# Kernel tuning notes

Measured on AMD Instinct MI355X. Metric: run time of the kernel, lower is better.

## Reference

```python
import jax, jax.numpy as jnp
import numpy as np

NEG = -1.0e9  # masked_fill value from the original module

def setup_inputs() -> dict:
    key = jax.random.key(0)
    kq, kk, kv, km = jax.random.split(key, 4)
    B, H, S, D = 4, 16, 2048, 64
    Q = jax.random.normal(kq, (B, H, S, D), dtype=jnp.float32)
    K = jax.random.normal(kk, (B, H, S, D), dtype=jnp.float32)
    V = jax.random.normal(kv, (B, H, S, D), dtype=jnp.float32)
    # boolean mask, True = masked out (broadcast over batch and heads)
    mask = jax.random.randint(km, (1, 1, S, S), 0, 2).astype(jnp.bool_)
    return {"Q": Q, "K": K, "V": V, "mask": mask}

def reference(Q, K, V, mask):
    d_k = K.shape[-1]
    scale = 1.0 / jnp.sqrt(jnp.asarray(d_k, dtype=Q.dtype))
    # [B,H,S,S] attention scores
    scores = jnp.einsum("bhqd,bhkd->bhqk", Q, K) * scale
    scores = jnp.where(mask, jnp.asarray(NEG, dtype=scores.dtype), scores)
    weights = jax.nn.softmax(scores, axis=-1)
    # dropout is identity in eval mode (self.training == False)
    return jnp.einsum("bhqk,bhkd->bhqd", weights, V)
```

## Files before the change

kernel.cpp:

```cpp
#include <hip/hip_runtime.h>
#include <stdint.h>

#define SQ 2048
#define DH 64

typedef __attribute__((ext_vector_type(8))) short bf16x8;
typedef __attribute__((ext_vector_type(4))) short bf16x4;
typedef __attribute__((ext_vector_type(4))) float f32x4;

static __device__ __forceinline__ unsigned short f2bf_rne(float x) {
  union { float f; uint32_t u; } v; v.f = x;
  uint32_t u = v.u;
  return (unsigned short)((u + 0x7FFFu + ((u >> 16) & 1u)) >> 16);
}

static __device__ __forceinline__ uint32_t pack_hi(float a, float b) {
  uint32_t au = __float_as_uint(a), bu = __float_as_uint(b);
#if __has_builtin(__builtin_amdgcn_perm)
  return __builtin_amdgcn_perm(bu, au, 0x07060302u);
#else
  return (bu & 0xFFFF0000u) | (au >> 16);
#endif
}

static __device__ __forceinline__ uint32_t pack_sel(float a, float b, uint32_t sel) {
#if __has_builtin(__builtin_amdgcn_perm)
  return __builtin_amdgcn_perm(__float_as_uint(b), __float_as_uint(a), sel);
#else
  uint32_t r = 0;
  uint64_t src = ((uint64_t)__float_as_uint(b) << 32) | __float_as_uint(a);
  for (int i = 0; i < 4; ++i) {
    uint32_t sb = (sel >> (8 * i)) & 0xFF;
    uint32_t byte = (sb < 8) ? (uint32_t)((src >> (8 * sb)) & 0xFF) : 0u;
    r |= byte << (8 * i);
  }
  return r;
#endif
}

static __device__ __forceinline__ float fast_exp2(float x) {
#if __has_builtin(__builtin_amdgcn_exp2f)
  return __builtin_amdgcn_exp2f(x);
#else
  return exp2f(x);
#endif
}

#if __has_builtin(__builtin_amdgcn_mfma_f32_16x16x16_bf16)
#define MFMA_PV(a, b, c) __builtin_amdgcn_mfma_f32_16x16x16_bf16((a), (b), (c), 0, 0, 0)
#else
#define MFMA_PV(a, b, c) __builtin_amdgcn_mfma_f32_16x16x16bf16_1k((a), (b), (c), 0, 0, 0)
#endif

__global__ __launch_bounds__(256) void pack_all(const float* __restrict__ K,
                                                const float* __restrict__ V,
                                                const int* __restrict__ mask,
                                                uint4* __restrict__ pk,
                                                uint2* __restrict__ pv,
                                                uint2* __restrict__ pm) {
  const int t = threadIdx.x;
  if (blockIdx.x < 2048) {
    __shared__ uint32_t Vw[64][33];
    const int bt = blockIdx.x;
    {
      const float* src = K + (size_t)bt * 64 * DH;
      uint4* dst = pk + (size_t)bt * 512;
#pragma unroll
      for (int j = 0; j < 2; ++j) {
        int i = t + j * 256;
        int kk = i >> 3, cp = i & 7;
        int c = cp ^ (kk & 7);
        const float4* s4 = (const float4*)(src + (size_t)kk * DH + c * 8);
        float4 a = s4[0], b = s4[1];
        uint4 w;
        w.x = pack_hi(a.x, a.y); w.y = pack_hi(a.z, a.w);
        w.z = pack_hi(b.x, b.y); w.w = pack_hi(b.z, b.w);
        dst[i] = w;
      }
    }
    {
      const float* src = V + (size_t)bt * 64 * DH;
#pragma unroll
      for (int half = 0; half < 2; ++half) {
        int kp = (t >> 4) + half * 16;
        int d4 = (t & 15) * 4;
        float4 a = *(const float4*)(src + (size_t)(2 * kp) * DH + d4);
        float4 b = *(const float4*)(src + (size_t)(2 * kp + 1) * DH + d4);
        Vw[d4 + 0][kp] = pack_hi(a.x, b.x);
        Vw[d4 + 1][kp] = pack_hi(a.y, b.y);
        Vw[d4 + 2][kp] = pack_hi(a.z, b.z);
        Vw[d4 + 3][kp] = pack_hi(a.w, b.w);
      }
      __syncthreads();
      uint2* dst = pv + (size_t)bt * 1024;
#pragma unroll
      for (int j = 0; j < 4; ++j) {
        int o = t + j * 256;
        int d = o >> 4, up = o & 15;
        int u = up ^ (d & 15);
        uint2 w;
        w.x = Vw[d][2 * u]; w.y = Vw[d][2 * u + 1];
        dst[o] = w;
      }
    }
  } else {
    __shared__ uint2 Lm[16][17];
    const int bid = blockIdx.x - 2048;
    const int qb = bid >> 5, gb = bid & 31;
    {
      int qq = t >> 4, gg = t & 15;
      int4 m = *(const int4*)(mask + (size_t)(qb * 16 + qq) * SQ + (gb * 64 + gg * 4));
      uint2 w;
      w.x = (m.x ? 0x00000C0Cu : 0x00000302u) | (m.y ? 0x0C0C0000u : 0x07060000u);
      w.y = (m.z ? 0x00000C0Cu : 0x00000302u) | (m.w ? 0x0C0C0000u : 0x07060000u);
      Lm[gg][qq] = w;
    }
    __syncthreads();
    {
      int gg = t >> 4, qq = t & 15;
      pm[(size_t)(gb * 16 + gg) * 2048 + qb * 16 + qq] = Lm[gg][qq];
    }
  }
}

__global__ void pack_mask_kernel(const int* __restrict__ mask,
                                 unsigned long long* __restrict__ bits) {
  const int lane = threadIdx.x & 63;
  const int gw = (blockIdx.x * blockDim.x + threadIdx.x) >> 6;
  const int nw = (gridDim.x * blockDim.x) >> 6;
  for (int w = gw; w < SQ * SQ / 64; w += nw) {
    int v = mask[(size_t)w * 64 + lane];
    unsigned long long b = __ballot(v != 0);
    if (lane == 0) bits[(size_t)(w & 31) * SQ + (w >> 5)] = b;
  }
}

__global__ __launch_bounds__(256, 2) void attn3(
    const uint4* __restrict__ pk, const uint4* __restrict__ pv,
    const uint2* __restrict__ pm, const float* __restrict__ Qg,
    float* __restrict__ Og) {
  __shared__ __align__(16) uint8_t smem[32768];

  const int id = blockIdx.x;
  const int bh = id & 63;
  const int qblk = id >> 6;
  const int t = threadIdx.x;
  const int wave = t >> 6, lane = t & 63, col = lane & 15, quad = lane >> 4;

  const float* Qb = Qg + (size_t)bh * SQ * DH;
  float* Ob = Og + (size_t)bh * SQ * DH;
  const uint4* pkb = pk + (size_t)bh * 32 * 512;
  const uint4* pvb = pv + (size_t)bh * 32 * 512;
  const int q0 = qblk * 256 + wave * 64;

  const float QSCALE = 0.18033688011112042f;
  bf16x8 qf[4][2];
#pragma unroll
  for (int s = 0; s < 4; ++s) {
    int q = q0 + s * 16 + col;
#pragma unroll
    for (int j = 0; j < 2; ++j) {
      const float4* p = (const float4*)(Qb + (size_t)q * DH + j * 32 + quad * 8);
      float4 a = p[0], b = p[1];
      bf16x8 f;
      f[0] = (short)f2bf_rne(a.x * QSCALE); f[1] = (short)f2bf_rne(a.y * QSCALE);
      f[2] = (short)f2bf_rne(a.z * QSCALE); f[3] = (short)f2bf_rne(a.w * QSCALE);
      f[4] = (short)f2bf_rne(b.x * QSCALE); f[5] = (short)f2bf_rne(b.y * QSCALE);
      f[6] = (short)f2bf_rne(b.z * QSCALE); f[7] = (short)f2bf_rne(b.w * QSCALE);
      qf[s][j] = f;
    }
  }

  const unsigned ka0 = col * 128 + ((quad ^ (col & 7)) * 16);
  const unsigned ka1 = col * 128 + (((4 + quad) ^ (col & 7)) * 16);
  unsigned va[4];
#pragma unroll
  for (int kt = 0; kt < 4; ++kt)
    va[kt] = 16384u + col * 128 + (((kt * 4 + quad) ^ col) * 8);
  const unsigned stK = t * 16;
  const unsigned stV = 16384u + t * 16;
  const char* pmt = (const char*)pm + (size_t)(quad * 2048 + q0 + col) * 8;

  f32x4 acc[4][4];
  f32x4 accl[4];
#pragma unroll
  for (int s = 0; s < 4; ++s) {
#pragma unroll
    for (int dt = 0; dt < 4; ++dt)
#pragma unroll
      for (int r = 0; r < 4; ++r) acc[s][dt][r] = 0.0f;
#pragma unroll
    for (int r = 0; r < 4; ++r) accl[s][r] = 0.0f;
  }
  bf16x4 vones;
  vones[0] = (short)0x3F80; vones[1] = (short)0x3F80;
  vones[2] = (short)0x3F80; vones[3] = (short)0x3F80;
  const f32x4 fz = {0.0f, 0.0f, 0.0f, 0.0f};

  {
    uint4 k0 = pkb[t], k1 = pkb[t + 256];
    uint4 v0 = pvb[t], v1 = pvb[t + 256];
    *(uint4*)(smem + stK) = k0; *(uint4*)(smem + stK + 4096) = k1;
    *(uint4*)(smem + stV) = v0; *(uint4*)(smem + stV + 4096) = v1;
  }
  unsigned buf = 0;

  for (int tile = 0; tile < 32; ++tile) {
    __syncthreads();
    const int tn = (tile < 31) ? tile + 1 : 31;

    const uint4* pkt = pkb + (size_t)tn * 512;
    const uint4* pvt = pvb + (size_t)tn * 512;
    uint4 k0 = pkt[t], k1 = pkt[t + 256];
    uint4 v0 = pvt[t], v1 = pvt[t + 256];

#pragma unroll
    for (int kt = 0; kt < 4; ++kt) {
      const bf16x8 kf0 = *(const bf16x8*)(smem + buf + kt * 2048 + ka0);
      const bf16x8 kf1 = *(const bf16x8*)(smem + buf + kt * 2048 + ka1);
      uint2 mw[4];
#pragma unroll
      for (int s = 0; s < 4; ++s)
        mw[s] = *(const uint2*)(pmt + (size_t)kt * 65536 + s * 128);

      uint32_t pf[4][2];
#pragma unroll
      for (int s = 0; s < 4; ++s) {
        f32x4 st = __builtin_amdgcn_mfma_f32_16x16x32_bf16(kf0, qf[s][0], fz, 0, 0, 0);
        st = __builtin_amdgcn_mfma_f32_16x16x32_bf16(kf1, qf[s][1], st, 0, 0, 0);
        float p0 = fast_exp2(st[0]), p1 = fast_exp2(st[1]);
        float p2 = fast_exp2(st[2]), p3 = fast_exp2(st[3]);
        pf[s][0] = pack_sel(p0, p1, mw[s].x);
        pf[s][1] = pack_sel(p2, p3, mw[s].y);
      }

      union { uint2 u2; bf16x4 v; } vf[4];
#pragma unroll
      for (int dt = 0; dt < 4; ++dt)
        vf[dt].u2 = *(const uint2*)(smem + buf + va[kt] + dt * 2048);
#pragma unroll
      for (int s = 0; s < 4; ++s) {
        union { uint32_t u[2]; bf16x4 v; } pw;
        pw.u[0] = pf[s][0]; pw.u[1] = pf[s][1];
        accl[s] = MFMA_PV(vones, pw.v, accl[s]);
#pragma unroll
        for (int dt = 0; dt < 4; ++dt)
          acc[s][dt] = MFMA_PV(vf[dt].v, pw.v, acc[s][dt]);
      }
    }

    const unsigned ob = buf ^ 8192u;
    *(uint4*)(smem + ob + stK) = k0; *(uint4*)(smem + ob + stK + 4096) = k1;
    *(uint4*)(smem + ob + stV) = v0; *(uint4*)(smem + ob + stV + 4096) = v1;
    buf = ob;
    pmt += 262144;
  }

#pragma unroll
  for (int s = 0; s < 4; ++s) {
    float inv = 1.0f / accl[s][0];
    int q = q0 + s * 16 + col;
    float* orow = Ob + (size_t)q * DH;
#pragma unroll
    for (int dt = 0; dt < 4; ++dt) {
      float4 o;
      o.x = acc[s][dt][0] * inv;
      o.y = acc[s][dt][1] * inv;
      o.z = acc[s][dt][2] * inv;
      o.w = acc[s][dt][3] * inv;
      *(float4*)(orow + dt * 16 + quad * 4) = o;
    }
  }
}

__global__ __launch_bounds__(512, 4) void attn_fb(
    const float* __restrict__ Qg, const float* __restrict__ Kg,
    const float* __restrict__ Vg, const unsigned long long* __restrict__ mbits,
    const int* __restrict__ mraw, float* __restrict__ Og) {
  __shared__ __align__(16) unsigned short Klds[2][64][72];
  __shared__ __align__(16) uint32_t Vtlds[2][64][36];
  const int id = blockIdx.x;
  const int bh = id & 63;
  const int qblk = id >> 6;
  const int t = threadIdx.x;
  const int wave = t >> 6, lane = t & 63, col = lane & 15, quad = lane >> 4;
  const float* Qb = Qg + (size_t)bh * SQ * DH;
  const float* Kb = Kg + (size_t)bh * SQ * DH;
  const float* Vb = Vg + (size_t)bh * SQ * DH;
  float* Ob = Og + (size_t)bh * SQ * DH;
  const int q0 = qblk * 256 + wave * 32;
  const int skk = t >> 3, sd8 = (t & 7) * 8, skp = t >> 4, sd4 = (t & 15) * 4;
  const float QSCALE = 0.18033688011112042f;
  bf16x8 qf[2][2];
#pragma unroll
  for (int s = 0; s < 2; ++s) {
    int q = q0 + s * 16 + col;
#pragma unroll
    for (int j = 0; j < 2; ++j) {
      const float4* p = (const float4*)(Qb + (size_t)q * DH + j * 32 + quad * 8);
      float4 a = p[0], b = p[1];
      bf16x8 f;
      f[0] = (short)f2bf_rne(a.x * QSCALE); f[1] = (short)f2bf_rne(a.y * QSCALE);
      f[2] = (short)f2bf_rne(a.z * QSCALE); f[3] = (short)f2bf_rne(a.w * QSCALE);
      f[4] = (short)f2bf_rne(b.x * QSCALE); f[5] = (short)f2bf_rne(b.y * QSCALE);
      f[6] = (short)f2bf_rne(b.z * QSCALE); f[7] = (short)f2bf_rne(b.w * QSCALE);
      qf[s][j] = f;
    }
  }
  f32x4 acc[2][4]; f32x4 accl[2];
#pragma unroll
  for (int s = 0; s < 2; ++s) {
#pragma unroll
    for (int dt = 0; dt < 4; ++dt)
#pragma unroll
      for (int r = 0; r < 4; ++r) acc[s][dt][r] = 0.0f;
#pragma unroll
    for (int r = 0; r < 4; ++r) accl[s][r] = 0.0f;
  }
  bf16x4 vones;
  vones[0] = (short)0x3F80; vones[1] = (short)0x3F80;
  vones[2] = (short)0x3F80; vones[3] = (short)0x3F80;
  const f32x4 fz = {0.0f, 0.0f, 0.0f, 0.0f};
  auto load_mask = [&](int ti, unsigned long long m[2]) {
    if (mbits) {
#pragma unroll
      for (int s = 0; s < 2; ++s)
        m[s] = mbits[(size_t)ti * SQ + (q0 + s * 16 + col)];
    } else {
#pragma unroll
      for (int s = 0; s < 2; ++s) {
        int q = q0 + s * 16 + col;
        unsigned long long mm = 0;
#pragma unroll
        for (int j = 0; j < 4; ++j) {
          int4 mi = *(const int4*)(mraw + (size_t)q * SQ + ti * 64 + j * 16 + quad * 4);
          unsigned long long nib = (unsigned long long)((mi.x != 0) | ((mi.y != 0) << 1) |
                                                        ((mi.z != 0) << 2) | ((mi.w != 0) << 3));
          mm |= nib << (j * 16 + quad * 4);
        }
        m[s] = mm;
      }
    }
  };
  {
    const float4* kp = (const float4*)(Kb + (size_t)skk * DH + sd8);
    float4 k0 = kp[0], k1 = kp[1];
    const float* va = Vb + (size_t)(skp * 2) * DH + sd4;
    float4 v0 = *(const float4*)va, v1 = *(const float4*)(va + DH);
    uint4 kw;
    kw.x = pack_hi(k0.x, k0.y); kw.y = pack_hi(k0.z, k0.w);
    kw.z = pack_hi(k1.x, k1.y); kw.w = pack_hi(k1.z, k1.w);
    *(uint4*)&Klds[0][skk][sd8] = kw;
    Vtlds[0][sd4 + 0][skp] = pack_hi(v0.x, v1.x);
    Vtlds[0][sd4 + 1][skp] = pack_hi(v0.y, v1.y);
    Vtlds[0][sd4 + 2][skp] = pack_hi(v0.z, v1.z);
    Vtlds[0][sd4 + 3][skp] = pack_hi(v0.w, v1.w);
  }
  unsigned long long mcur[2];
  load_mask(0, mcur);
  for (int tile = 0; tile < 32; ++tile) {
    __syncthreads();
    const int cb = tile & 1, nb = cb ^ 1;
    const int tn = (tile + 1 < 32) ? tile + 1 : tile;
    const int kkn = tn * 64;
    const float4* kp = (const float4*)(Kb + (size_t)(kkn + skk) * DH + sd8);
    float4 k0 = kp[0], k1 = kp[1];
    const float* va = Vb + (size_t)(kkn + skp * 2) * DH + sd4;
    float4 v0 = *(const float4*)va;
    float4 v1 = *(const float4*)(va + DH);
    unsigned long long mnxt[2];
    load_mask(tn, mnxt);
    uint32_t pfw[2][4][2];
#pragma unroll
    for (int kt = 0; kt < 4; ++kt) {
      const bf16x8 kf0 = *(const bf16x8*)&Klds[cb][kt * 16 + col][quad * 8];
      const bf16x8 kf1 = *(const bf16x8*)&Klds[cb][kt * 16 + col][32 + quad * 8];
#pragma unroll
      for (int s = 0; s < 2; ++s) {
        f32x4 st = __builtin_amdgcn_mfma_f32_16x16x32_bf16(kf0, qf[s][0], fz, 0, 0, 0);
        st = __builtin_amdgcn_mfma_f32_16x16x32_bf16(kf1, qf[s][1], st, 0, 0, 0);
        uint32_t nib = (uint32_t)(mcur[s] >> (kt * 16 + quad * 4)) & 0xFu;
        float p[4];
#pragma unroll
        for (int r = 0; r < 4; ++r)
          p[r] = fast_exp2(((nib >> r) & 1u) ? -1.0e9f : st[r]);
        pfw[s][kt][0] = pack_hi(p[0], p[1]);
        pfw[s][kt][1] = pack_hi(p[2], p[3]);
      }
    }
    {
      uint4 kw;
      kw.x = pack_hi(k0.x, k0.y); kw.y = pack_hi(k0.z, k0.w);
      kw.z = pack_hi(k1.x, k1.y); kw.w = pack_hi(k1.z, k1.w);
      *(uint4*)&Klds[nb][skk][sd8] = kw;
      Vtlds[nb][sd4 + 0][skp] = pack_hi(v0.x, v1.x);
      Vtlds[nb][sd4 + 1][skp] = pack_hi(v0.y, v1.y);
      Vtlds[nb][sd4 + 2][skp] = pack_hi(v0.z, v1.z);
      Vtlds[nb][sd4 + 3][skp] = pack_hi(v0.w, v1.w);
    }
    mcur[0] = mnxt[0]; mcur[1] = mnxt[1];
#pragma unroll
    for (int kt = 0; kt < 4; ++kt) {
      union { uint32_t u[2]; bf16x4 v; } p0, p1;
      p0.u[0] = pfw[0][kt][0]; p0.u[1] = pfw[0][kt][1];
      p1.u[0] = pfw[1][kt][0]; p1.u[1] = pfw[1][kt][1];
      accl[0] = MFMA_PV(vones, p0.v, accl[0]);
      accl[1] = MFMA_PV(vones, p1.v, accl[1]);
#pragma unroll
      for (int dt = 0; dt < 4; ++dt) {
        union { uint2 u2; bf16x4 v; } cv;
        cv.u2 = *(const uint2*)&Vtlds[cb][dt * 16 + col][kt * 8 + quad * 2];
        acc[0][dt] = MFMA_PV(cv.v, p0.v, acc[0][dt]);
        acc[1][dt] = MFMA_PV(cv.v, p1.v, acc[1][dt]);
      }
    }
  }
#pragma unroll
  for (int s = 0; s < 2; ++s) {
    float inv = 1.0f / accl[s][0];
    int q = q0 + s * 16 + col;
    float* orow = Ob + (size_t)q * DH;
#pragma unroll
    for (int dt = 0; dt < 4; ++dt) {
      float4 o;
      o.x = acc[s][dt][0] * inv;
      o.y = acc[s][dt][1] * inv;
      o.z = acc[s][dt][2] * inv;
      o.w = acc[s][dt][3] * inv;
      *(float4*)(orow + dt * 16 + quad * 4) = o;
    }
  }
}

extern "C" void kernel_launch(void* const* d_in, const int* in_sizes, int n_in,
                              void* d_out, int out_size, void* d_ws, size_t ws_size,
                              hipStream_t stream) {
  const float* Q = (const float*)d_in[0];
  const float* K = (const float*)d_in[1];
  const float* V = (const float*)d_in[2];
  const int* mask = (const int*)d_in[3];
  float* out = (float*)d_out;

  const size_t PK_BYTES = (size_t)64 * 32 * 8192;
  const size_t PV_BYTES = (size_t)64 * 32 * 8192;
  const size_t PM_BYTES = (size_t)512 * 2048 * 8;
  const size_t NEED = PK_BYTES + PV_BYTES + PM_BYTES;

  if (ws_size >= NEED) {
    uint4* pk = (uint4*)d_ws;
    uint2* pv = (uint2*)((char*)d_ws + PK_BYTES);
    uint2* pm = (uint2*)((char*)d_ws + PK_BYTES + PV_BYTES);
    pack_all<<<6144, 256, 0, stream>>>(K, V, mask, pk, pv, pm);
    attn3<<<512, 256, 0, stream>>>(pk, (uint4*)pv, pm, Q, out);
  } else if (ws_size >= (size_t)SQ * SQ / 8) {
    unsigned long long* bits = (unsigned long long*)d_ws;
    pack_mask_kernel<<<1024, 256, 0, stream>>>(mask, bits);
    attn_fb<<<512, 512, 0, stream>>>(Q, K, V, bits, mask, out);
  } else {
    attn_fb<<<512, 512, 0, stream>>>(Q, K, V, nullptr, mask, out);
  }
}
```

Measured before the change: 244.7 us.

## Halve queries per wave and stream K/V tiles directly into LDS

```diff
diff --git a/kernel.cpp b/kernel.cpp
--- a/kernel.cpp
+++ b/kernel.cpp
@@ -51,6 +51,16 @@
 #else
 #define MFMA_PV(a, b, c) __builtin_amdgcn_mfma_f32_16x16x16bf16_1k((a), (b), (c), 0, 0, 0)
 #endif
+
+typedef __attribute__((address_space(1))) const void as1_const_void;
+typedef __attribute__((address_space(3))) void as3_void;
+static __device__ __forceinline__ void gload_lds16(const void* g, void* l, int lane) {
+#if __has_builtin(__builtin_amdgcn_global_load_lds)
+  __builtin_amdgcn_global_load_lds((as1_const_void*)g, (as3_void*)l, 16, 0, 0);
+#else
+  *(uint4*)((char*)l + lane * 16) = *(const uint4*)g;
+#endif
+}
 
 __global__ __launch_bounds__(256) void pack_all(const float* __restrict__ K,
                                                 const float* __restrict__ V,
@@ -135,7 +145,7 @@
   }
 }
 
-__global__ __launch_bounds__(256, 2) void attn3(
+__global__ __launch_bounds__(256, 4) void attn3(
     const uint4* __restrict__ pk, const uint4* __restrict__ pv,
     const uint2* __restrict__ pm, const float* __restrict__ Qg,
     float* __restrict__ Og) {
@@ -151,12 +161,12 @@
   float* Ob = Og + (size_t)bh * SQ * DH;
   const uint4* pkb = pk + (size_t)bh * 32 * 512;
   const uint4* pvb = pv + (size_t)bh * 32 * 512;
-  const int q0 = qblk * 256 + wave * 64;
+  const int q0 = qblk * 128 + wave * 32;
 
   const float QSCALE = 0.18033688011112042f;
-  bf16x8 qf[4][2];
-#pragma unroll
-  for (int s = 0; s < 4; ++s) {
+  bf16x8 qf[2][2];
+#pragma unroll
+  for (int s = 0; s < 2; ++s) {
     int q = q0 + s * 16 + col;
 #pragma unroll
     for (int j = 0; j < 2; ++j) {
@@ -177,14 +187,12 @@
 #pragma unroll
   for (int kt = 0; kt < 4; ++kt)
     va[kt] = 16384u + col * 128 + (((kt * 4 + quad) ^ col) * 8);
-  const unsigned stK = t * 16;
-  const unsigned stV = 16384u + t * 16;
   const char* pmt = (const char*)pm + (size_t)(quad * 2048 + q0 + col) * 8;
 
-  f32x4 acc[4][4];
-  f32x4 accl[4];
-#pragma unroll
-  for (int s = 0; s < 4; ++s) {
+  f32x4 acc[2][4];
+  f32x4 accl[2];
+#pragma unroll
+  for (int s = 0; s < 2; ++s) {
 #pragma unroll
     for (int dt = 0; dt < 4; ++dt)
 #pragma unroll
@@ -197,35 +205,36 @@
   vones[2] = (short)0x3F80; vones[3] = (short)0x3F80;
   const f32x4 fz = {0.0f, 0.0f, 0.0f, 0.0f};
 
-  {
-    uint4 k0 = pkb[t], k1 = pkb[t + 256];
-    uint4 v0 = pvb[t], v1 = pvb[t + 256];
-    *(uint4*)(smem + stK) = k0; *(uint4*)(smem + stK + 4096) = k1;
-    *(uint4*)(smem + stV) = v0; *(uint4*)(smem + stV + 4096) = v1;
-  }
+  gload_lds16(pkb + t,       smem + wave * 1024,         lane);
+  gload_lds16(pkb + t + 256, smem + 4096 + wave * 1024,  lane);
+  gload_lds16(pvb + t,       smem + 16384 + wave * 1024, lane);
+  gload_lds16(pvb + t + 256, smem + 20480 + wave * 1024, lane);
   unsigned buf = 0;
 
   for (int tile = 0; tile < 32; ++tile) {
     __syncthreads();
     const int tn = (tile < 31) ? tile + 1 : 31;
+    const unsigned ob = buf ^ 8192u;
 
     const uint4* pkt = pkb + (size_t)tn * 512;
     const uint4* pvt = pvb + (size_t)tn * 512;
-    uint4 k0 = pkt[t], k1 = pkt[t + 256];
-    uint4 v0 = pvt[t], v1 = pvt[t + 256];
+    gload_lds16(pkt + t,       smem + ob + wave * 1024,         lane);
+    gload_lds16(pkt + t + 256, smem + ob + 4096 + wave * 1024,  lane);
+    gload_lds16(pvt + t,       smem + ob + 16384 + wave * 1024, lane);
+    gload_lds16(pvt + t + 256, smem + ob + 20480 + wave * 1024, lane);
 
 #pragma unroll
     for (int kt = 0; kt < 4; ++kt) {
       const bf16x8 kf0 = *(const bf16x8*)(smem + buf + kt * 2048 + ka0);
       const bf16x8 kf1 = *(const bf16x8*)(smem + buf + kt * 2048 + ka1);
-      uint2 mw[4];
-#pragma unroll
-      for (int s = 0; s < 4; ++s)
+      uint2 mw[2];
+#pragma unroll
+      for (int s = 0; s < 2; ++s)
         mw[s] = *(const uint2*)(pmt + (size_t)kt * 65536 + s * 128);
 
-      uint32_t pf[4][2];
-#pragma unroll
-      for (int s = 0; s < 4; ++s) {
+      uint32_t pf[2][2];
+#pragma unroll
+      for (int s = 0; s < 2; ++s) {
         f32x4 st = __builtin_amdgcn_mfma_f32_16x16x32_bf16(kf0, qf[s][0], fz, 0, 0, 0);
         st = __builtin_amdgcn_mfma_f32_16x16x32_bf16(kf1, qf[s][1], st, 0, 0, 0);
         float p0 = fast_exp2(st[0]), p1 = fast_exp2(st[1]);
@@ -234,30 +243,26 @@
         pf[s][1] = pack_sel(p2, p3, mw[s].y);
       }
 
-      union { uint2 u2; bf16x4 v; } vf[4];
-#pragma unroll
-      for (int dt = 0; dt < 4; ++dt)
-        vf[dt].u2 = *(const uint2*)(smem + buf + va[kt] + dt * 2048);
-#pragma unroll
-      for (int s = 0; s < 4; ++s) {
-        union { uint32_t u[2]; bf16x4 v; } pw;
-        pw.u[0] = pf[s][0]; pw.u[1] = pf[s][1];
-        accl[s] = MFMA_PV(vones, pw.v, accl[s]);
-#pragma unroll
-        for (int dt = 0; dt < 4; ++dt)
-          acc[s][dt] = MFMA_PV(vf[dt].v, pw.v, acc[s][dt]);
-      }
-    }
-
-    const unsigned ob = buf ^ 8192u;
-    *(uint4*)(smem + ob + stK) = k0; *(uint4*)(smem + ob + stK + 4096) = k1;
-    *(uint4*)(smem + ob + stV) = v0; *(uint4*)(smem + ob + stV + 4096) = v1;
+      union { uint32_t u[2]; bf16x4 v; } pw0, pw1;
+      pw0.u[0] = pf[0][0]; pw0.u[1] = pf[0][1];
+      pw1.u[0] = pf[1][0]; pw1.u[1] = pf[1][1];
+      accl[0] = MFMA_PV(vones, pw0.v, accl[0]);
+      accl[1] = MFMA_PV(vones, pw1.v, accl[1]);
+#pragma unroll
+      for (int dt = 0; dt < 4; ++dt) {
+        union { uint2 u2; bf16x4 v; } vf;
+        vf.u2 = *(const uint2*)(smem + buf + va[kt] + dt * 2048);
+        acc[0][dt] = MFMA_PV(vf.v, pw0.v, acc[0][dt]);
+        acc[1][dt] = MFMA_PV(vf.v, pw1.v, acc[1][dt]);
+      }
+    }
+
     buf = ob;
     pmt += 262144;
   }
 
 #pragma unroll
-  for (int s = 0; s < 4; ++s) {
+  for (int s = 0; s < 2; ++s) {
     float inv = 1.0f / accl[s][0];
     int q = q0 + s * 16 + col;
     float* orow = Ob + (size_t)q * DH;
@@ -451,7 +456,7 @@
     uint2* pv = (uint2*)((char*)d_ws + PK_BYTES);
     uint2* pm = (uint2*)((char*)d_ws + PK_BYTES + PV_BYTES);
     pack_all<<<6144, 256, 0, stream>>>(K, V, mask, pk, pv, pm);
-    attn3<<<512, 256, 0, stream>>>(pk, (uint4*)pv, pm, Q, out);
+    attn3<<<1024, 256, 0, stream>>>(pk, (uint4*)pv, pm, Q, out);
   } else if (ws_size >= (size_t)SQ * SQ / 8) {
     unsigned long long* bits = (unsigned long long*)d_ws;
     pack_mask_kernel<<<1024, 256, 0, stream>>>(mask, bits);
```

Measured after the change: 239.9 us (median of 2 runs). About the same (-1.9%).
